# Optimization experiments

Measured on AMD Instinct MI355X. Metric: run time of the kernel, lower is better.

The kernel has to match this reference:

```python
import jax, jax.numpy as jnp
import numpy as np

N = 524288
D = 256
NUM_SEG = 4096

def setup_inputs() -> dict:
    key = jax.random.key(0)
    k1, k2, k3 = jax.random.split(key, 3)
    node_features = jax.random.normal(k1, (N, D), dtype=jnp.float32)
    batch_index = jnp.sort(jax.random.randint(k2, (N,), 0, NUM_SEG, dtype=jnp.int64))
    W = jax.random.normal(k3, (D, 1), dtype=jnp.float32) / np.sqrt(D)
    b = jnp.zeros((1,), dtype=jnp.float32)
    return {"node_features": node_features, "batch_index": batch_index,
            "num_segments": NUM_SEG, "W": W, "b": b}

def reference(node_features, batch_index, num_segments, W, b):
    # scores: [N, 1] linear projection
    scores = node_features @ W + b
    # softmax over dim=0 (global across all nodes, matching the torch code)
    attn = jax.nn.softmax(scores, axis=0)  # [N, 1]
    weighted = node_features * attn        # [N, D]
    pooled = jax.ops.segment_sum(weighted, batch_index, num_segments=num_segments)
    return pooled
```

## Files before the change

### kernel.cpp

```cpp
#include <hip/hip_runtime.h>

#define D 256
#define NODES_PER_WAVE 64

__global__ __launch_bounds__(256) void attn_pool_fused(
    const float* __restrict__ x, const int* __restrict__ idx,
    const float* __restrict__ W, const float* __restrict__ bias_p,
    float* __restrict__ out, float* __restrict__ zsum, int N) {
  const int tid  = blockIdx.x * blockDim.x + threadIdx.x;
  const int wave = tid >> 6;
  const int lane = threadIdx.x & 63;
  const long start = (long)wave * NODES_PER_WAVE;
  if (start >= N) return;
  const int count = (int)min((long)NODES_PER_WAVE, (long)N - start);

  const float4 w4 = reinterpret_cast<const float4*>(W)[lane];
  const float bias = *bias_p;

  int nidx = (start + lane < N) ? idx[start + lane] : idx[N - 1];

  float4 acc = make_float4(0.f, 0.f, 0.f, 0.f);
  int cur_seg = __shfl(nidx, 0);
  float zpart = 0.f;

  for (int i = 0; i < count; ++i) {
    const float4 x4 =
        reinterpret_cast<const float4*>(x + (start + i) * (long)D)[lane];
    float s = x4.x * w4.x + x4.y * w4.y + x4.z * w4.z + x4.w * w4.w;
#pragma unroll
    for (int o = 1; o < 64; o <<= 1) s += __shfl_xor(s, o);
    s += bias;
    const float e = expf(s);
    zpart += e;

    const int seg = __shfl(nidx, i);
    if (seg != cur_seg) {
      float* op = out + (long)cur_seg * D + lane * 4;
      atomicAdd(op + 0, acc.x);
      atomicAdd(op + 1, acc.y);
      atomicAdd(op + 2, acc.z);
      atomicAdd(op + 3, acc.w);
      acc = make_float4(0.f, 0.f, 0.f, 0.f);
      cur_seg = seg;
    }
    acc.x += e * x4.x;
    acc.y += e * x4.y;
    acc.z += e * x4.z;
    acc.w += e * x4.w;
  }
  float* op = out + (long)cur_seg * D + lane * 4;
  atomicAdd(op + 0, acc.x);
  atomicAdd(op + 1, acc.y);
  atomicAdd(op + 2, acc.z);
  atomicAdd(op + 3, acc.w);
  if (lane == 0) atomicAdd(zsum, zpart);
}

__global__ __launch_bounds__(256) void attn_pool_scale(
    float* __restrict__ out, const float* __restrict__ zsum, int n4) {
  const int i = blockIdx.x * blockDim.x + threadIdx.x;
  if (i >= n4) return;
  const float inv = 1.0f / *zsum;
  float4 v = reinterpret_cast<float4*>(out)[i];
  v.x *= inv; v.y *= inv; v.z *= inv; v.w *= inv;
  reinterpret_cast<float4*>(out)[i] = v;
}

extern "C" void kernel_launch(void* const* d_in, const int* in_sizes, int n_in,
                              void* d_out, int out_size, void* d_ws, size_t ws_size,
                              hipStream_t stream) {
  const float* x   = (const float*)d_in[0];
  const int*   idx = (const int*)d_in[1];
  const float* W   = (const float*)d_in[3];
  const float* b   = (const float*)d_in[4];
  float* out  = (float*)d_out;
  float* zsum = (float*)d_ws;

  const int N = in_sizes[1];

  hipMemsetAsync(out, 0, (size_t)out_size * sizeof(float), stream);
  hipMemsetAsync(zsum, 0, sizeof(float), stream);

  const int num_waves = (N + NODES_PER_WAVE - 1) / NODES_PER_WAVE;
  const int block = 256;
  const int grid = (num_waves * 64 + block - 1) / block;
  attn_pool_fused<<<grid, block, 0, stream>>>(x, idx, W, b, out, zsum, N);

  const int n4 = out_size / 4;
  attn_pool_scale<<<(n4 + block - 1) / block, block, 0, stream>>>(out, zsum, n4);
}
```

Measured before the change: 777.9 us.

## Software-pipeline row loads and batch four reductions per iteration in attention pooling

Restructures the main loop to process four rows per step. The next four rows are prefetched with nontemporal loads while the current ones are computed, and the four wave reductions are interleaved to expose more independent work. Segment boundaries are found upfront with a ballot bitmask instead of a shuffle per row. The softmax denominator partials are combined per block in shared memory, so each block issues one atomic instead of one per wave. This costs more registers (launch bounds set to 4 blocks) and duplicates the tail path for partial waves.

```diff
diff --git a/kernel.cpp b/kernel.cpp
--- a/kernel.cpp
+++ b/kernel.cpp
@@ -1,59 +1,107 @@
 #include <hip/hip_runtime.h>
 
 #define D 256
-#define NODES_PER_WAVE 64
+#define NPW 64
 
-__global__ __launch_bounds__(256) void attn_pool_fused(
+typedef float vf4 __attribute__((ext_vector_type(4)));
+
+__global__ __launch_bounds__(256, 4) void attn_pool_fused(
     const float* __restrict__ x, const int* __restrict__ idx,
     const float* __restrict__ W, const float* __restrict__ bias_p,
     float* __restrict__ out, float* __restrict__ zsum, int N) {
   const int tid  = blockIdx.x * blockDim.x + threadIdx.x;
   const int wave = tid >> 6;
   const int lane = threadIdx.x & 63;
-  const long start = (long)wave * NODES_PER_WAVE;
-  if (start >= N) return;
-  const int count = (int)min((long)NODES_PER_WAVE, (long)N - start);
+  const long start = (long)wave * NPW;
+  const bool active = start < N;
 
-  const float4 w4 = reinterpret_cast<const float4*>(W)[lane];
-  const float bias = *bias_p;
-
-  int nidx = (start + lane < N) ? idx[start + lane] : idx[N - 1];
-
-  float4 acc = make_float4(0.f, 0.f, 0.f, 0.f);
-  int cur_seg = __shfl(nidx, 0);
+  __shared__ float zs[4];
   float zpart = 0.f;
 
-  for (int i = 0; i < count; ++i) {
-    const float4 x4 =
-        reinterpret_cast<const float4*>(x + (start + i) * (long)D)[lane];
-    float s = x4.x * w4.x + x4.y * w4.y + x4.z * w4.z + x4.w * w4.w;
+  if (active) {
+    const float4 w4 = reinterpret_cast<const float4*>(W)[lane];
+    const float bias = *bias_p;
+    const int count = (int)min((long)NPW, (long)N - start);
+
+    int nidx = idx[min(start + (long)lane, (long)N - 1)];
+    const int prev = __shfl_up(nidx, 1);
+    const unsigned long long chg = __ballot(lane > 0 && nidx != prev);
+
+    const vf4* xrow = reinterpret_cast<const vf4*>(x) + start * (D / 4) + lane;
+
+    int cur_seg = __shfl(nidx, 0);
+    float ax = 0.f, ay = 0.f, az = 0.f, aw = 0.f;
+
+    auto flushacc = [&](void) {
+      float* op = out + (long)cur_seg * D + lane * 4;
+      atomicAdd(op + 0, ax);
+      atomicAdd(op + 1, ay);
+      atomicAdd(op + 2, az);
+      atomicAdd(op + 3, aw);
+      ax = ay = az = aw = 0.f;
+    };
+
+    if (count == NPW) {
+      auto process4 = [&](int b, vf4 c0, vf4 c1, vf4 c2, vf4 c3) {
+        float s0 = c0[0] * w4.x + c0[1] * w4.y + c0[2] * w4.z + c0[3] * w4.w;
+        float s1 = c1[0] * w4.x + c1[1] * w4.y + c1[2] * w4.z + c1[3] * w4.w;
+        float s2 = c2[0] * w4.x + c2[1] * w4.y + c2[2] * w4.z + c2[3] * w4.w;
+        float s3 = c3[0] * w4.x + c3[1] * w4.y + c3[2] * w4.z + c3[3] * w4.w;
 #pragma unroll
-    for (int o = 1; o < 64; o <<= 1) s += __shfl_xor(s, o);
-    s += bias;
-    const float e = expf(s);
-    zpart += e;
+        for (int o = 1; o < 64; o <<= 1) {
+          s0 += __shfl_xor(s0, o);
+          s1 += __shfl_xor(s1, o);
+          s2 += __shfl_xor(s2, o);
+          s3 += __shfl_xor(s3, o);
+        }
+        const float e0 = expf(s0 + bias);
+        const float e1 = expf(s1 + bias);
+        const float e2 = expf(s2 + bias);
+        const float e3 = expf(s3 + bias);
+        zpart += (e0 + e1) + (e2 + e3);
+        if (chg & (1ull << (b + 0))) { flushacc(); cur_seg = __shfl(nidx, b + 0); }
+        ax += e0 * c0[0]; ay += e0 * c0[1]; az += e0 * c0[2]; aw += e0 * c0[3];
+        if (chg & (1ull << (b + 1))) { flushacc(); cur_seg = __shfl(nidx, b + 1); }
+        ax += e1 * c1[0]; ay += e1 * c1[1]; az += e1 * c1[2]; aw += e1 * c1[3];
+        if (chg & (1ull << (b + 2))) { flushacc(); cur_seg = __shfl(nidx, b + 2); }
+        ax += e2 * c2[0]; ay += e2 * c2[1]; az += e2 * c2[2]; aw += e2 * c2[3];
+        if (chg & (1ull << (b + 3))) { flushacc(); cur_seg = __shfl(nidx, b + 3); }
+        ax += e3 * c3[0]; ay += e3 * c3[1]; az += e3 * c3[2]; aw += e3 * c3[3];
+      };
 
-    const int seg = __shfl(nidx, i);
-    if (seg != cur_seg) {
-      float* op = out + (long)cur_seg * D + lane * 4;
-      atomicAdd(op + 0, acc.x);
-      atomicAdd(op + 1, acc.y);
-      atomicAdd(op + 2, acc.z);
-      atomicAdd(op + 3, acc.w);
-      acc = make_float4(0.f, 0.f, 0.f, 0.f);
-      cur_seg = seg;
+      vf4 c0 = __builtin_nontemporal_load(xrow + 0 * (D / 4));
+      vf4 c1 = __builtin_nontemporal_load(xrow + 1 * (D / 4));
+      vf4 c2 = __builtin_nontemporal_load(xrow + 2 * (D / 4));
+      vf4 c3 = __builtin_nontemporal_load(xrow + 3 * (D / 4));
+      for (int g = 0; g < 15; ++g) {
+        const vf4* p = xrow + (long)(g + 1) * 4 * (D / 4);
+        vf4 n0 = __builtin_nontemporal_load(p + 0 * (D / 4));
+        vf4 n1 = __builtin_nontemporal_load(p + 1 * (D / 4));
+        vf4 n2 = __builtin_nontemporal_load(p + 2 * (D / 4));
+        vf4 n3 = __builtin_nontemporal_load(p + 3 * (D / 4));
+        process4(g * 4, c0, c1, c2, c3);
+        c0 = n0; c1 = n1; c2 = n2; c3 = n3;
+      }
+      process4(60, c0, c1, c2, c3);
+      flushacc();
+    } else {
+      for (int i = 0; i < count; ++i) {
+        const vf4 xi = xrow[(long)i * (D / 4)];
+        float s = xi[0] * w4.x + xi[1] * w4.y + xi[2] * w4.z + xi[3] * w4.w;
+#pragma unroll
+        for (int o = 1; o < 64; o <<= 1) s += __shfl_xor(s, o);
+        const float e = expf(s + bias);
+        zpart += e;
+        if (i > 0 && (chg & (1ull << i))) { flushacc(); cur_seg = __shfl(nidx, i); }
+        ax += e * xi[0]; ay += e * xi[1]; az += e * xi[2]; aw += e * xi[3];
+      }
+      flushacc();
     }
-    acc.x += e * x4.x;
-    acc.y += e * x4.y;
-    acc.z += e * x4.z;
-    acc.w += e * x4.w;
   }
-  float* op = out + (long)cur_seg * D + lane * 4;
-  atomicAdd(op + 0, acc.x);
-  atomicAdd(op + 1, acc.y);
-  atomicAdd(op + 2, acc.z);
-  atomicAdd(op + 3, acc.w);
-  if (lane == 0) atomicAdd(zsum, zpart);
+
+  if (lane == 0) zs[threadIdx.x >> 6] = zpart;
+  __syncthreads();
+  if (threadIdx.x == 0) atomicAdd(zsum, (zs[0] + zs[1]) + (zs[2] + zs[3]));
 }
 
 __global__ __launch_bounds__(256) void attn_pool_scale(
@@ -81,7 +129,7 @@
   hipMemsetAsync(out, 0, (size_t)out_size * sizeof(float), stream);
   hipMemsetAsync(zsum, 0, sizeof(float), stream);
 
-  const int num_waves = (N + NODES_PER_WAVE - 1) / NODES_PER_WAVE;
+  const int num_waves = (N + NPW - 1) / NPW;
   const int block = 256;
   const int grid = (num_waves * 64 + block - 1) / block;
   attn_pool_fused<<<grid, block, 0, stream>>>(x, idx, W, b, out, zsum, N);
```

After: 675.9 us. -13.1%, faster.
